# Optimization experiments

Hardware: AMD Instinct MI355X
Metric: run time of the kernel (lower is better)

The kernel has to match this reference:

```python
import jax, jax.numpy as jnp
from jax import lax
import numpy as np

D_MODEL = 1024
D_STATE = 16
D_CONV = 4
EXPAND = 2
D_INNER = EXPAND * D_MODEL          # 2048
DT_RANK = (D_MODEL + 15) // 16      # 64
B_SZ, SEQ = 2, 2048


def setup_inputs() -> dict:
    key = jax.random.key(0)
    ks = jax.random.split(key, 10)
    s = 0.02
    x = jax.random.normal(ks[0], (B_SZ, SEQ, D_MODEL), jnp.float32)
    ln_w = jnp.ones((D_MODEL,), jnp.float32)
    ln_b = jnp.zeros((D_MODEL,), jnp.float32)
    in_proj_w = jax.random.normal(ks[1], (2 * D_INNER, D_MODEL), jnp.float32) * s
    conv_w = jax.random.normal(ks[2], (D_INNER, 1, D_CONV), jnp.float32) * s
    conv_b = jnp.zeros((D_INNER,), jnp.float32)
    x_proj_w = jax.random.normal(ks[3], (DT_RANK + 2 * D_STATE, D_INNER), jnp.float32) * s
    dt_proj_w = jax.random.normal(ks[4], (D_INNER, DT_RANK), jnp.float32) * s
    dt_proj_b = jax.random.normal(ks[5], (D_INNER,), jnp.float32) * s
    # standard Mamba S4D-real init: A = -[1..d_state] per channel
    A_log = jnp.log(jnp.tile(jnp.arange(1, D_STATE + 1, dtype=jnp.float32), (D_INNER, 1)))
    D_param = jnp.ones((D_INNER,), jnp.float32)
    out_proj_w = jax.random.normal(ks[6], (D_MODEL, D_INNER), jnp.float32) * s
    return dict(x=x, ln_w=ln_w, ln_b=ln_b, in_proj_w=in_proj_w, conv_w=conv_w,
                conv_b=conv_b, x_proj_w=x_proj_w, dt_proj_w=dt_proj_w,
                dt_proj_b=dt_proj_b, A_log=A_log, D_param=D_param,
                out_proj_w=out_proj_w)


def _mamba_layer(x, ln_w, ln_b, in_proj_w, conv_w, conv_b, x_proj_w,
                 dt_proj_w, dt_proj_b, A_log, D_param, out_proj_w):
    # LayerNorm (eps=1e-5)
    mu = x.mean(-1, keepdims=True)
    var = ((x - mu) ** 2).mean(-1, keepdims=True)
    xn = (x - mu) * lax.rsqrt(var + 1e-5) * ln_w + ln_b

    # input projection -> gate + conv branch
    xz = jnp.einsum('bld,ed->ble', xn, in_proj_w)  # [B,L,2*D_INNER]
    x_in, z = jnp.split(xz, 2, axis=-1)

    # causal depthwise conv1d + SiLU
    xc = lax.conv_general_dilated(x_in.transpose(0, 2, 1), conv_w, (1,),
                                  [(D_CONV - 1, 0)],
                                  dimension_numbers=('NCH', 'OIH', 'NCH'),
                                  feature_group_count=D_INNER)
    xc = jax.nn.silu(xc + conv_b[None, :, None]).transpose(0, 2, 1)  # [B,L,D_INNER]

    # SSM parameters
    dbl = jnp.einsum('bld,ed->ble', xc, x_proj_w)  # [B,L,DT_RANK+2N]
    dt, Bm, Cm = jnp.split(dbl, [DT_RANK, DT_RANK + D_STATE], axis=-1)
    delta = jax.nn.softplus(jnp.einsum('blr,dr->bld', dt, dt_proj_w) + dt_proj_b)
    A = -jnp.exp(A_log)  # [D_INNER, D_STATE]

    # selective scan over time
    def step(h, inp):
        d_t, B_t, C_t, u_t = inp  # [B,D_INNER],[B,N],[B,N],[B,D_INNER]
        dA = jnp.exp(d_t[..., None] * A)                         # [B,D_INNER,N]
        h = dA * h + (d_t * u_t)[..., None] * B_t[:, None, :]    # [B,D_INNER,N]
        y = jnp.einsum('bdn,bn->bd', h, C_t)
        return h, y

    h0 = jnp.zeros((x.shape[0], D_INNER, D_STATE), x.dtype)
    _, ys = lax.scan(step, h0, (delta.transpose(1, 0, 2), Bm.transpose(1, 0, 2),
                                Cm.transpose(1, 0, 2), xc.transpose(1, 0, 2)))
    y = ys.transpose(1, 0, 2) + xc * D_param   # [B,L,D_INNER]

    y = y * jax.nn.silu(z)
    out = jnp.einsum('ble,de->bld', y, out_proj_w)
    # dropout p=0 (eval) -> identity; residual
    return x + out


def reference(x, ln_w, ln_b, in_proj_w, conv_w, conv_b, x_proj_w,
              dt_proj_w, dt_proj_b, A_log, D_param, out_proj_w):
    return _mamba_layer(x, ln_w, ln_b, in_proj_w, conv_w, conv_b, x_proj_w,
                        dt_proj_w, dt_proj_b, A_log, D_param, out_proj_w)
```

## Files before the change

### kernel.cpp

```cpp
#include <hip/hip_runtime.h>
#include <hip/hip_bf16.h>
#include <math.h>

#define D_MODEL 1024
#define D_INNER 2048
#define DT_RANK 64
#define D_STATE 16
#define BSZ 2
#define SEQ 2048
#define NROW (BSZ * SEQ)
#define NC 128
#define CL (SEQ / NC)
#define NCH (BSZ * D_INNER)
#define KSPLIT 16
#define KCH (D_INNER / KSPLIT)

typedef short bf16x8 __attribute__((ext_vector_type(8)));
typedef float f32x4 __attribute__((ext_vector_type(4)));

__device__ inline ushort f2bf(float f) {
    uint32_t u = __float_as_uint(f);
    return (ushort)((u + 0x7FFFu + ((u >> 16) & 1u)) >> 16);
}
__device__ inline float bf2f(ushort u) {
    return __uint_as_float(((uint32_t)u) << 16);
}

__device__ inline void gld_lds16(const void* g, void* l) {
    __builtin_amdgcn_global_load_lds(
        (__attribute__((address_space(1))) void*)g,
        (__attribute__((address_space(3))) void*)l, 16, 0, 0);
}

__global__ __launch_bounds__(256) void cvt_bf16(const float* __restrict__ in,
                                                ushort* __restrict__ out) {
    int i = blockIdx.x * 256 + threadIdx.x;
    float4 v = ((const float4*)in)[i];
    ushort4 o;
    o.x = f2bf(v.x); o.y = f2bf(v.y); o.z = f2bf(v.z); o.w = f2bf(v.w);
    ((ushort4*)out)[i] = o;
}

__global__ __launch_bounds__(256) void ln_kernel(const float* __restrict__ x,
                                                 const float* __restrict__ w,
                                                 const float* __restrict__ b,
                                                 ushort* __restrict__ xn) {
    int row = blockIdx.x;
    int tid = threadIdx.x;
    const float4* xr = (const float4*)(x + (size_t)row * D_MODEL);
    float4 v = xr[tid];
    float s  = v.x + v.y + v.z + v.w;
    float ss = v.x * v.x + v.y * v.y + v.z * v.z + v.w * v.w;
#pragma unroll
    for (int o = 32; o > 0; o >>= 1) {
        s  += __shfl_down(s, o);
        ss += __shfl_down(ss, o);
    }
    __shared__ float red[8];
    int wid = tid >> 6, lane = tid & 63;
    if (lane == 0) { red[wid] = s; red[4 + wid] = ss; }
    __syncthreads();
    s  = red[0] + red[1] + red[2] + red[3];
    ss = red[4] + red[5] + red[6] + red[7];
    float mu  = s * (1.0f / D_MODEL);
    float var = ss * (1.0f / D_MODEL) - mu * mu;
    float inv = rsqrtf(var + 1e-5f);
    float4 wv = ((const float4*)w)[tid];
    float4 bv = ((const float4*)b)[tid];
    ushort4 o4;
    o4.x = f2bf((v.x - mu) * inv * wv.x + bv.x);
    o4.y = f2bf((v.y - mu) * inv * wv.y + bv.y);
    o4.z = f2bf((v.z - mu) * inv * wv.z + bv.z);
    o4.w = f2bf((v.w - mu) * inv * wv.w + bv.w);
    ((ushort4*)(xn + (size_t)row * D_MODEL))[tid] = o4;
}

template <int MODE>
__global__ __launch_bounds__(256) void gemm_mfma(
    const ushort* __restrict__ A, int lda,
    const ushort* __restrict__ B, int ldb,
    float* __restrict__ C, ushort* __restrict__ Zb, int ldc, int splitN,
    const float* __restrict__ extra, int K) {
    __shared__ ushort lds[2][2][128 * 32];
    int tid = threadIdx.x;
    int w = tid >> 6, lane = tid & 63;
    int bm = blockIdx.y * 128, bn = blockIdx.x * 128;
    int wr = w >> 1, wc = w & 1;

    int srow = tid >> 2, sseg = (tid & 3) << 3;
    const ushort* Abase = A + (size_t)(bm + srow) * lda + sseg;
    const ushort* Bbase = B + (size_t)(bn + srow) * ldb + sseg;
    int l0 = w * 512;

    int frow = lane & 15, fk = (lane >> 4) << 3;
    f32x4 acc[4][4] = {};

#define STAGE(buf, k0)                                                        \
    do {                                                                      \
        gld_lds16(Abase + (k0),                     &lds[buf][0][l0]);        \
        gld_lds16(Abase + (size_t)64 * lda + (k0),  &lds[buf][0][2048 + l0]); \
        gld_lds16(Bbase + (k0),                     &lds[buf][1][l0]);        \
        gld_lds16(Bbase + (size_t)64 * ldb + (k0),  &lds[buf][1][2048 + l0]); \
    } while (0)

    int nk = K >> 5;
    int cur = 0;
    STAGE(0, 0);
    __syncthreads();
    for (int kt = 0; kt < nk; ++kt) {
        if (kt + 1 < nk) STAGE(cur ^ 1, (kt + 1) << 5);
        bf16x8 a[4], b[4];
#pragma unroll
        for (int m = 0; m < 4; ++m)
            a[m] = *(const bf16x8*)&lds[cur][0][(wr * 64 + m * 16 + frow) * 32 + fk];
#pragma unroll
        for (int n = 0; n < 4; ++n)
            b[n] = *(const bf16x8*)&lds[cur][1][(wc * 64 + n * 16 + frow) * 32 + fk];
#pragma unroll
        for (int m = 0; m < 4; ++m)
#pragma unroll
            for (int n = 0; n < 4; ++n)
                acc[m][n] = __builtin_amdgcn_mfma_f32_16x16x32_bf16(a[m], b[n], acc[m][n], 0, 0, 0);
        __syncthreads();
        cur ^= 1;
    }
#undef STAGE

    int rbase = bm + wr * 64 + ((lane >> 4) << 2);
    int cbase = bn + wc * 64 + (lane & 15);
#pragma unroll
    for (int m = 0; m < 4; ++m) {
#pragma unroll
        for (int n = 0; n < 4; ++n) {
            int gc = cbase + n * 16;
#pragma unroll
            for (int j = 0; j < 4; ++j) {
                int gr = rbase + m * 16 + j;
                float v = acc[m][n][j];
                if (MODE == 0) {
                    if (gc < splitN) C[(size_t)gr * ldc + gc] = v;
                    else             Zb[(size_t)gr * ldc + (gc - splitN)] = f2bf(v);
                } else {
                    C[(size_t)gr * ldc + gc] = v + extra[(size_t)gr * ldc + gc];
                }
            }
        }
    }
}

#define BM 64
#define BN 64
#define BK 16
template <int MODE>
__global__ __launch_bounds__(256) void gemm_tn(const float* __restrict__ A, int lda,
                                               const float* __restrict__ B, int ldb,
                                               float* __restrict__ C, int ldc,
                                               int M, int N, int K,
                                               const float* __restrict__ extra) {
    __shared__ float As[BK][BM];
    __shared__ float Bs[BK][BN];
    int bm = blockIdx.y * BM, bn = blockIdx.x * BN;
    int tid = threadIdx.x;
    int tx = tid & 15, ty = tid >> 4;
    int lrow = tid >> 2, lseg = (tid & 3) << 2;
    float acc[4][4] = {};

    for (int k0 = 0; k0 < K; k0 += BK) {
        float4 av = make_float4(0.f, 0.f, 0.f, 0.f);
        float4 bv = make_float4(0.f, 0.f, 0.f, 0.f);
        int agr = bm + lrow;
        if (agr < M) av = *(const float4*)(A + (size_t)agr * lda + k0 + lseg);
        int bgr = bn + lrow;
        if (bgr < N) bv = *(const float4*)(B + (size_t)bgr * ldb + k0 + lseg);
        __syncthreads();
        As[lseg + 0][lrow] = av.x; As[lseg + 1][lrow] = av.y;
        As[lseg + 2][lrow] = av.z; As[lseg + 3][lrow] = av.w;
        Bs[lseg + 0][lrow] = bv.x; Bs[lseg + 1][lrow] = bv.y;
        Bs[lseg + 2][lrow] = bv.z; Bs[lseg + 3][lrow] = bv.w;
        __syncthreads();
#pragma unroll
        for (int k = 0; k < BK; ++k) {
            float4 a4 = *(const float4*)&As[k][ty << 2];
            float4 b4 = *(const float4*)&Bs[k][tx << 2];
            float ar[4] = {a4.x, a4.y, a4.z, a4.w};
            float br[4] = {b4.x, b4.y, b4.z, b4.w};
#pragma unroll
            for (int i = 0; i < 4; ++i)
#pragma unroll
                for (int j = 0; j < 4; ++j) acc[i][j] += ar[i] * br[j];
        }
    }

#pragma unroll
    for (int i = 0; i < 4; ++i) {
        int gr = bm + (ty << 2) + i;
        if (gr >= M) continue;
#pragma unroll
        for (int j = 0; j < 4; ++j) {
            int gc = bn + (tx << 2) + j;
            if (gc >= N) continue;
            float v = acc[i][j];
            if (MODE == 1) {
                v += extra[gc];
                v = (v > 20.f) ? v : log1pf(expf(v));
                C[(size_t)gr * ldc + gc] = v;
            } else {
                C[(size_t)gr * ldc + gc] = v;
            }
        }
    }
}

__global__ __launch_bounds__(256) void gemm_b_split(const float* __restrict__ A,
                                                    const float* __restrict__ B,
                                                    float* __restrict__ part) {
    __shared__ float As[BK][BM];
    __shared__ float Bs[BK][BN];
    int bm = blockIdx.y * BM, bn = blockIdx.x * BN;
    int kc = blockIdx.z;
    int tid = threadIdx.x;
    int tx = tid & 15, ty = tid >> 4;
    int lrow = tid >> 2, lseg = (tid & 3) << 2;
    float acc[4][4] = {};

    int kbeg = kc * KCH;
    for (int k0 = kbeg; k0 < kbeg + KCH; k0 += BK) {
        float4 av = *(const float4*)(A + (size_t)(bm + lrow) * D_INNER + k0 + lseg);
        float4 bv = make_float4(0.f, 0.f, 0.f, 0.f);
        int bgr = bn + lrow;
        if (bgr < 96) bv = *(const float4*)(B + (size_t)bgr * D_INNER + k0 + lseg);
        __syncthreads();
        As[lseg + 0][lrow] = av.x; As[lseg + 1][lrow] = av.y;
        As[lseg + 2][lrow] = av.z; As[lseg + 3][lrow] = av.w;
        Bs[lseg + 0][lrow] = bv.x; Bs[lseg + 1][lrow] = bv.y;
        Bs[lseg + 2][lrow] = bv.z; Bs[lseg + 3][lrow] = bv.w;
        __syncthreads();
#pragma unroll
        for (int k = 0; k < BK; ++k) {
            float4 a4 = *(const float4*)&As[k][ty << 2];
            float4 b4 = *(const float4*)&Bs[k][tx << 2];
            float ar[4] = {a4.x, a4.y, a4.z, a4.w};
            float br[4] = {b4.x, b4.y, b4.z, b4.w};
#pragma unroll
            for (int i = 0; i < 4; ++i)
#pragma unroll
                for (int j = 0; j < 4; ++j) acc[i][j] += ar[i] * br[j];
        }
    }

    float* po = part + (size_t)kc * (NROW * 96);
#pragma unroll
    for (int i = 0; i < 4; ++i) {
        int gr = bm + (ty << 2) + i;
#pragma unroll
        for (int j = 0; j < 4; ++j) {
            int gc = bn + (tx << 2) + j;
            if (gc < 96) po[(size_t)gr * 96 + gc] = acc[i][j];
        }
    }
}

__global__ __launch_bounds__(256) void gemm_b_reduce(const float* __restrict__ part,
                                                     float* __restrict__ dbl) {
    int i = blockIdx.x * 256 + threadIdx.x;
    float s = 0.f;
#pragma unroll
    for (int kc = 0; kc < KSPLIT; ++kc)
        s += part[(size_t)kc * (NROW * 96) + i];
    dbl[i] = s;
}

__global__ __launch_bounds__(256) void conv_silu(const float* __restrict__ xin,
                                                 const float* __restrict__ w,
                                                 const float* __restrict__ cb,
                                                 float* __restrict__ xc) {
    int idx = blockIdx.x * 256 + threadIdx.x;
    int d4 = idx & 511;
    int m  = idx >> 9;
    int l  = m & (SEQ - 1);
    int d  = d4 << 2;
    float4 w0 = ((const float4*)w)[d + 0];
    float4 w1 = ((const float4*)w)[d + 1];
    float4 w2 = ((const float4*)w)[d + 2];
    float4 w3 = ((const float4*)w)[d + 3];
    float wr0[4] = {w0.x, w0.y, w0.z, w0.w};
    float wr1[4] = {w1.x, w1.y, w1.z, w1.w};
    float wr2[4] = {w2.x, w2.y, w2.z, w2.w};
    float wr3[4] = {w3.x, w3.y, w3.z, w3.w};
    float ax = cb[d], ay = cb[d + 1], az = cb[d + 2], aw = cb[d + 3];
#pragma unroll
    for (int j = 0; j < 4; ++j) {
        if (l - 3 + j >= 0) {
            float4 xv = *(const float4*)(xin + (size_t)(m - 3 + j) * D_INNER + d);
            ax += wr0[j] * xv.x;
            ay += wr1[j] * xv.y;
            az += wr2[j] * xv.z;
            aw += wr3[j] * xv.w;
        }
    }
    float4 o;
    o.x = ax / (1.f + __expf(-ax));
    o.y = ay / (1.f + __expf(-ay));
    o.z = az / (1.f + __expf(-az));
    o.w = aw / (1.f + __expf(-aw));
    *(float4*)(xc + (size_t)m * D_INNER + d) = o;
}

#define EXP4(e, cj) \
    e.x = __expf(dt * cj.x); e.y = __expf(dt * cj.y); \
    e.z = __expf(dt * cj.z); e.w = __expf(dt * cj.w);
#define HUPD(hj, cj, Bv) { float4 e; EXP4(e, cj) \
    hj.x = e.x * hj.x + du * Bv.x; hj.y = e.y * hj.y + du * Bv.y; \
    hj.z = e.z * hj.z + du * Bv.z; hj.w = e.w * hj.w + du * Bv.w; }

__global__ __launch_bounds__(256) void scan_phase1(const float* __restrict__ delta,
                                                   const float* __restrict__ xc,
                                                   const float* __restrict__ dbl,
                                                   const float* __restrict__ A_log,
                                                   float* __restrict__ S,
                                                   float* __restrict__ sumdt) {
    __shared__ float bs[CL][16];
    int tid = threadIdx.x;
    int g = blockIdx.x * 256 + tid;
    int c = g & (NCH - 1);
    int k = g >> 12;
    int d = c & (D_INNER - 1);
    int b = c >> 11;
    size_t r0 = (size_t)b * SEQ + (size_t)k * CL;

    if (tid < CL * 4) {
        int t = tid >> 2, j = (tid & 3) << 2;
        *(float4*)&bs[t][j] = *(const float4*)(dbl + (r0 + t) * 96 + DT_RANK + j);
    }

    const float4* al = (const float4*)(A_log + d * D_STATE);
    float4 c0 = al[0], c1 = al[1], c2 = al[2], c3 = al[3];
    c0.x = -__expf(c0.x); c0.y = -__expf(c0.y); c0.z = -__expf(c0.z); c0.w = -__expf(c0.w);
    c1.x = -__expf(c1.x); c1.y = -__expf(c1.y); c1.z = -__expf(c1.z); c1.w = -__expf(c1.w);
    c2.x = -__expf(c2.x); c2.y = -__expf(c2.y); c2.z = -__expf(c2.z); c2.w = -__expf(c2.w);
    c3.x = -__expf(c3.x); c3.y = -__expf(c3.y); c3.z = -__expf(c3.z); c3.w = -__expf(c3.w);
    __syncthreads();

    const float* pd = delta + r0 * D_INNER + d;
    const float* pu = xc    + r0 * D_INNER + d;
    float4 h0 = {}, h1 = {}, h2 = {}, h3 = {};
    float sdt = 0.f;
#pragma unroll 4
    for (int t = 0; t < CL; ++t) {
        float dt = *pd, u = *pu;
        float4 B0 = *(const float4*)&bs[t][0];
        float4 B1 = *(const float4*)&bs[t][4];
        float4 B2 = *(const float4*)&bs[t][8];
        float4 B3 = *(const float4*)&bs[t][12];
        float du = dt * u;
        sdt += dt;
        HUPD(h0, c0, B0) HUPD(h1, c1, B1) HUPD(h2, c2, B2) HUPD(h3, c3, B3)
        pd += D_INNER; pu += D_INNER;
    }
    float4* So = (float4*)(S + ((size_t)g << 4));
    So[0] = h0; So[1] = h1; So[2] = h2; So[3] = h3;
    sumdt[g] = sdt;
}

__global__ __launch_bounds__(256) void scan_phase2(float* __restrict__ S,
                                                   const float* __restrict__ sumdt,
                                                   const float* __restrict__ A_log) {
    int g = blockIdx.x * 256 + threadIdx.x;
    int n = g & 15;
    int c = g >> 4;
    int d = c & (D_INNER - 1);
    float cn = -__expf(A_log[d * D_STATE + n]);
    float h = 0.f;
#pragma unroll 8
    for (int k = 0; k < NC; ++k) {
        int kc = (k << 12) | c;
        float P = __expf(sumdt[kc] * cn);
        size_t o = ((size_t)kc << 4) + n;
        float s = S[o];
        S[o] = h;
        h = P * h + s;
    }
}

__global__ __launch_bounds__(256) void scan_phase3(const float* __restrict__ delta,
                                                   const float* __restrict__ xc,
                                                   const float* __restrict__ dbl,
                                                   const ushort* __restrict__ zb,
                                                   const float* __restrict__ A_log,
                                                   const float* __restrict__ Dp,
                                                   const float* __restrict__ hin,
                                                   ushort* __restrict__ y) {
    __shared__ float bcs[CL][32];
    int tid = threadIdx.x;
    int g = blockIdx.x * 256 + tid;
    int c = g & (NCH - 1);
    int k = g >> 12;
    int d = c & (D_INNER - 1);
    int b = c >> 11;
    size_t r0 = (size_t)b * SEQ + (size_t)k * CL;

    if (tid < CL * 8) {
        int t = tid >> 3, j = (tid & 7) << 2;
        *(float4*)&bcs[t][j] = *(const float4*)(dbl + (r0 + t) * 96 + DT_RANK + j);
    }

    const float4* al = (const float4*)(A_log + d * D_STATE);
    float4 c0 = al[0], c1 = al[1], c2 = al[2], c3 = al[3];
    c0.x = -__expf(c0.x); c0.y = -__expf(c0.y); c0.z = -__expf(c0.z); c0.w = -__expf(c0.w);
    c1.x = -__expf(c1.x); c1.y = -__expf(c1.y); c1.z = -__expf(c1.z); c1.w = -__expf(c1.w);
    c2.x = -__expf(c2.x); c2.y = -__expf(c2.y); c2.z = -__expf(c2.z); c2.w = -__expf(c2.w);
    c3.x = -__expf(c3.x); c3.y = -__expf(c3.y); c3.z = -__expf(c3.z); c3.w = -__expf(c3.w);
    float Dv = Dp[d];
    const float4* hi = (const float4*)(hin + ((size_t)g << 4));
    float4 h0 = hi[0], h1 = hi[1], h2 = hi[2], h3 = hi[3];
    __syncthreads();

    const float* pd = delta + r0 * D_INNER + d;
    const float* pu = xc    + r0 * D_INNER + d;
    const ushort* pz = zb   + r0 * D_INNER + d;
    ushort* py = y          + r0 * D_INNER + d;
#pragma unroll 4
    for (int t = 0; t < CL; ++t) {
        float dt = *pd, u = *pu;
        float4 B0 = *(const float4*)&bcs[t][0];
        float4 B1 = *(const float4*)&bcs[t][4];
        float4 B2 = *(const float4*)&bcs[t][8];
        float4 B3 = *(const float4*)&bcs[t][12];
        float4 C0 = *(const float4*)&bcs[t][16];
        float4 C1 = *(const float4*)&bcs[t][20];
        float4 C2 = *(const float4*)&bcs[t][24];
        float4 C3 = *(const float4*)&bcs[t][28];
        float du = dt * u;
        HUPD(h0, c0, B0) HUPD(h1, c1, B1) HUPD(h2, c2, B2) HUPD(h3, c3, B3)
        float acc = h0.x * C0.x + h0.y * C0.y + h0.z * C0.z + h0.w * C0.w
                  + h1.x * C1.x + h1.y * C1.y + h1.z * C1.z + h1.w * C1.w
                  + h2.x * C2.x + h2.y * C2.y + h2.z * C2.z + h2.w * C2.w
                  + h3.x * C3.x + h3.y * C3.y + h3.z * C3.z + h3.w * C3.w;
        float zv = bf2f(*pz);
        float sz = zv / (1.f + __expf(-zv));
        *py = f2bf((acc + u * Dv) * sz);
        pd += D_INNER; pu += D_INNER; pz += D_INNER; py += D_INNER;
    }
}

extern "C" void kernel_launch(void* const* d_in, const int* in_sizes, int n_in,
                              void* d_out, int out_size, void* d_ws, size_t ws_size,
                              hipStream_t stream) {
    const float* x       = (const float*)d_in[0];
    const float* ln_w    = (const float*)d_in[1];
    const float* ln_b    = (const float*)d_in[2];
    const float* in_proj = (const float*)d_in[3];
    const float* conv_w  = (const float*)d_in[4];
    const float* conv_b  = (const float*)d_in[5];
    const float* x_proj  = (const float*)d_in[6];
    const float* dt_w    = (const float*)d_in[7];
    const float* dt_b    = (const float*)d_in[8];
    const float* A_log   = (const float*)d_in[9];
    const float* Dp      = (const float*)d_in[10];
    const float* out_w   = (const float*)d_in[11];
    float* out = (float*)d_out;

    char* ws = (char*)d_ws;
    const size_t MB = 1024ull * 1024ull;
    ushort* xn_bf    = (ushort*)(ws);
    ushort* w_in_bf  = (ushort*)(ws + 8 * MB);
    float*  Shin     = (float*)(ws);
    float*  x_in     = (float*)(ws + 16 * MB);
    float*  part     = (float*)(ws + 16 * MB);
    ushort* w_out_bf = (ushort*)(ws + 41 * MB);
    float*  sumdt    = (float*)(ws + 45 * MB);
    ushort* zbuf_bf  = (ushort*)(ws + 48 * MB);
    float*  xc       = (float*)(ws + 64 * MB);
    float*  dbl      = (float*)(ws + 96 * MB);
    float*  delta    = (float*)(ws + 98 * MB);
    ushort* y_bf     = (ushort*)(ws + 130 * MB);

    cvt_bf16<<<(2 * D_INNER * D_MODEL / 4) / 256, 256, 0, stream>>>(in_proj, w_in_bf);

    ln_kernel<<<NROW, 256, 0, stream>>>(x, ln_w, ln_b, xn_bf);

    gemm_mfma<0><<<dim3(4096 / 128, NROW / 128), 256, 0, stream>>>(
        xn_bf, D_MODEL, w_in_bf, D_MODEL, x_in, zbuf_bf, D_INNER, D_INNER,
        nullptr, D_MODEL);

    conv_silu<<<(NROW * (D_INNER / 4)) / 256, 256, 0, stream>>>(x_in, conv_w, conv_b, xc);

    cvt_bf16<<<(D_MODEL * D_INNER / 4) / 256, 256, 0, stream>>>(out_w, w_out_bf);

    gemm_b_split<<<dim3(2, NROW / BM, KSPLIT), 256, 0, stream>>>(xc, x_proj, part);
    gemm_b_reduce<<<(NROW * 96) / 256, 256, 0, stream>>>(part, dbl);

    gemm_tn<1><<<dim3(D_INNER / BN, NROW / BM), 256, 0, stream>>>(
        dbl, 96, dt_w, DT_RANK, delta, D_INNER, NROW, D_INNER, DT_RANK, dt_b);

    scan_phase1<<<(NCH * NC) / 256, 256, 0, stream>>>(
        delta, xc, dbl, A_log, Shin, sumdt);
    scan_phase2<<<(NCH * D_STATE) / 256, 256, 0, stream>>>(Shin, sumdt, A_log);
    scan_phase3<<<(NCH * NC) / 256, 256, 0, stream>>>(
        delta, xc, dbl, zbuf_bf, A_log, Dp, Shin, y_bf);

    gemm_mfma<2><<<dim3(D_MODEL / 128, NROW / 128), 256, 0, stream>>>(
        y_bf, D_INNER, w_out_bf, D_INNER, out, nullptr, D_MODEL, 0,
        x, D_INNER);
}
```

Before: 408.6 us.

## Store intermediates in bf16 and move dt projection to MFMA GEMM

```diff
diff --git a/kernel.cpp b/kernel.cpp
--- a/kernel.cpp
+++ b/kernel.cpp
@@ -79,8 +79,8 @@
 __global__ __launch_bounds__(256) void gemm_mfma(
     const ushort* __restrict__ A, int lda,
     const ushort* __restrict__ B, int ldb,
-    float* __restrict__ C, ushort* __restrict__ Zb, int ldc, int splitN,
-    const float* __restrict__ extra, int K) {
+    float* __restrict__ C, ushort* __restrict__ Z0, ushort* __restrict__ Z1,
+    int ldc, int splitN, const float* __restrict__ extra, int K) {
     __shared__ ushort lds[2][2][128 * 32];
     int tid = threadIdx.x;
     int w = tid >> 6, lane = tid & 63;
@@ -138,8 +138,12 @@
                 int gr = rbase + m * 16 + j;
                 float v = acc[m][n][j];
                 if (MODE == 0) {
-                    if (gc < splitN) C[(size_t)gr * ldc + gc] = v;
-                    else             Zb[(size_t)gr * ldc + (gc - splitN)] = f2bf(v);
+                    if (gc < splitN) Z0[(size_t)gr * ldc + gc] = f2bf(v);
+                    else             Z1[(size_t)gr * ldc + (gc - splitN)] = f2bf(v);
+                } else if (MODE == 1) {
+                    v += extra[gc];
+                    v = (v > 20.f) ? v : log1pf(__expf(v));
+                    Z0[(size_t)gr * ldc + gc] = f2bf(v);
                 } else {
                     C[(size_t)gr * ldc + gc] = v + extra[(size_t)gr * ldc + gc];
                 }
@@ -151,67 +155,7 @@
 #define BM 64
 #define BN 64
 #define BK 16
-template <int MODE>
-__global__ __launch_bounds__(256) void gemm_tn(const float* __restrict__ A, int lda,
-                                               const float* __restrict__ B, int ldb,
-                                               float* __restrict__ C, int ldc,
-                                               int M, int N, int K,
-                                               const float* __restrict__ extra) {
-    __shared__ float As[BK][BM];
-    __shared__ float Bs[BK][BN];
-    int bm = blockIdx.y * BM, bn = blockIdx.x * BN;
-    int tid = threadIdx.x;
-    int tx = tid & 15, ty = tid >> 4;
-    int lrow = tid >> 2, lseg = (tid & 3) << 2;
-    float acc[4][4] = {};
-
-    for (int k0 = 0; k0 < K; k0 += BK) {
-        float4 av = make_float4(0.f, 0.f, 0.f, 0.f);
-        float4 bv = make_float4(0.f, 0.f, 0.f, 0.f);
-        int agr = bm + lrow;
-        if (agr < M) av = *(const float4*)(A + (size_t)agr * lda + k0 + lseg);
-        int bgr = bn + lrow;
-        if (bgr < N) bv = *(const float4*)(B + (size_t)bgr * ldb + k0 + lseg);
-        __syncthreads();
-        As[lseg + 0][lrow] = av.x; As[lseg + 1][lrow] = av.y;
-        As[lseg + 2][lrow] = av.z; As[lseg + 3][lrow] = av.w;
-        Bs[lseg + 0][lrow] = bv.x; Bs[lseg + 1][lrow] = bv.y;
-        Bs[lseg + 2][lrow] = bv.z; Bs[lseg + 3][lrow] = bv.w;
-        __syncthreads();
-#pragma unroll
-        for (int k = 0; k < BK; ++k) {
-            float4 a4 = *(const float4*)&As[k][ty << 2];
-            float4 b4 = *(const float4*)&Bs[k][tx << 2];
-            float ar[4] = {a4.x, a4.y, a4.z, a4.w};
-            float br[4] = {b4.x, b4.y, b4.z, b4.w};
-#pragma unroll
-            for (int i = 0; i < 4; ++i)
-#pragma unroll
-                for (int j = 0; j < 4; ++j) acc[i][j] += ar[i] * br[j];
-        }
-    }
-
-#pragma unroll
-    for (int i = 0; i < 4; ++i) {
-        int gr = bm + (ty << 2) + i;
-        if (gr >= M) continue;
-#pragma unroll
-        for (int j = 0; j < 4; ++j) {
-            int gc = bn + (tx << 2) + j;
-            if (gc >= N) continue;
-            float v = acc[i][j];
-            if (MODE == 1) {
-                v += extra[gc];
-                v = (v > 20.f) ? v : log1pf(expf(v));
-                C[(size_t)gr * ldc + gc] = v;
-            } else {
-                C[(size_t)gr * ldc + gc] = v;
-            }
-        }
-    }
-}
-
-__global__ __launch_bounds__(256) void gemm_b_split(const float* __restrict__ A,
+__global__ __launch_bounds__(256) void gemm_b_split(const ushort* __restrict__ A,
                                                     const float* __restrict__ B,
                                                     float* __restrict__ part) {
     __shared__ float As[BK][BM];
@@ -225,7 +169,8 @@
 
     int kbeg = kc * KCH;
     for (int k0 = kbeg; k0 < kbeg + KCH; k0 += BK) {
-        float4 av = *(const float4*)(A + (size_t)(bm + lrow) * D_INNER + k0 + lseg);
+        ushort4 au = *(const ushort4*)(A + (size_t)(bm + lrow) * D_INNER + k0 + lseg);
+        float4 av = make_float4(bf2f(au.x), bf2f(au.y), bf2f(au.z), bf2f(au.w));
         float4 bv = make_float4(0.f, 0.f, 0.f, 0.f);
         int bgr = bn + lrow;
         if (bgr < 96) bv = *(const float4*)(B + (size_t)bgr * D_INNER + k0 + lseg);
@@ -261,19 +206,19 @@
 }
 
 __global__ __launch_bounds__(256) void gemm_b_reduce(const float* __restrict__ part,
-                                                     float* __restrict__ dbl) {
+                                                     ushort* __restrict__ dbl) {
     int i = blockIdx.x * 256 + threadIdx.x;
     float s = 0.f;
 #pragma unroll
     for (int kc = 0; kc < KSPLIT; ++kc)
         s += part[(size_t)kc * (NROW * 96) + i];
-    dbl[i] = s;
-}
-
-__global__ __launch_bounds__(256) void conv_silu(const float* __restrict__ xin,
+    dbl[i] = f2bf(s);
+}
+
+__global__ __launch_bounds__(256) void conv_silu(const ushort* __restrict__ xin,
                                                  const float* __restrict__ w,
                                                  const float* __restrict__ cb,
-                                                 float* __restrict__ xc) {
+                                                 ushort* __restrict__ xc) {
     int idx = blockIdx.x * 256 + threadIdx.x;
     int d4 = idx & 511;
     int m  = idx >> 9;
@@ -291,19 +236,19 @@
 #pragma unroll
     for (int j = 0; j < 4; ++j) {
         if (l - 3 + j >= 0) {
-            float4 xv = *(const float4*)(xin + (size_t)(m - 3 + j) * D_INNER + d);
-            ax += wr0[j] * xv.x;
-            ay += wr1[j] * xv.y;
-            az += wr2[j] * xv.z;
-            aw += wr3[j] * xv.w;
+            ushort4 xu = *(const ushort4*)(xin + (size_t)(m - 3 + j) * D_INNER + d);
+            ax += wr0[j] * bf2f(xu.x);
+            ay += wr1[j] * bf2f(xu.y);
+            az += wr2[j] * bf2f(xu.z);
+            aw += wr3[j] * bf2f(xu.w);
         }
     }
-    float4 o;
-    o.x = ax / (1.f + __expf(-ax));
-    o.y = ay / (1.f + __expf(-ay));
-    o.z = az / (1.f + __expf(-az));
-    o.w = aw / (1.f + __expf(-aw));
-    *(float4*)(xc + (size_t)m * D_INNER + d) = o;
+    ushort4 o;
+    o.x = f2bf(ax / (1.f + __expf(-ax)));
+    o.y = f2bf(ay / (1.f + __expf(-ay)));
+    o.z = f2bf(az / (1.f + __expf(-az)));
+    o.w = f2bf(aw / (1.f + __expf(-aw)));
+    *(ushort4*)(xc + (size_t)m * D_INNER + d) = o;
 }
 
 #define EXP4(e, cj) \
@@ -313,9 +258,9 @@
     hj.x = e.x * hj.x + du * Bv.x; hj.y = e.y * hj.y + du * Bv.y; \
     hj.z = e.z * hj.z + du * Bv.z; hj.w = e.w * hj.w + du * Bv.w; }
 
-__global__ __launch_bounds__(256) void scan_phase1(const float* __restrict__ delta,
-                                                   const float* __restrict__ xc,
-                                                   const float* __restrict__ dbl,
+__global__ __launch_bounds__(256) void scan_phase1(const ushort* __restrict__ delta,
+                                                   const ushort* __restrict__ xc,
+                                                   const ushort* __restrict__ dbl,
                                                    const float* __restrict__ A_log,
                                                    float* __restrict__ S,
                                                    float* __restrict__ sumdt) {
@@ -330,7 +275,9 @@
 
     if (tid < CL * 4) {
         int t = tid >> 2, j = (tid & 3) << 2;
-        *(float4*)&bs[t][j] = *(const float4*)(dbl + (r0 + t) * 96 + DT_RANK + j);
+        ushort4 u4 = *(const ushort4*)(dbl + (r0 + t) * 96 + DT_RANK + j);
+        bs[t][j + 0] = bf2f(u4.x); bs[t][j + 1] = bf2f(u4.y);
+        bs[t][j + 2] = bf2f(u4.z); bs[t][j + 3] = bf2f(u4.w);
     }
 
     const float4* al = (const float4*)(A_log + d * D_STATE);
@@ -341,13 +288,13 @@
     c3.x = -__expf(c3.x); c3.y = -__expf(c3.y); c3.z = -__expf(c3.z); c3.w = -__expf(c3.w);
     __syncthreads();
 
-    const float* pd = delta + r0 * D_INNER + d;
-    const float* pu = xc    + r0 * D_INNER + d;
+    const ushort* pd = delta + r0 * D_INNER + d;
+    const ushort* pu = xc    + r0 * D_INNER + d;
     float4 h0 = {}, h1 = {}, h2 = {}, h3 = {};
     float sdt = 0.f;
 #pragma unroll 4
     for (int t = 0; t < CL; ++t) {
-        float dt = *pd, u = *pu;
+        float dt = bf2f(*pd), u = bf2f(*pu);
         float4 B0 = *(const float4*)&bs[t][0];
         float4 B1 = *(const float4*)&bs[t][4];
         float4 B2 = *(const float4*)&bs[t][8];
@@ -382,9 +329,9 @@
     }
 }
 
-__global__ __launch_bounds__(256) void scan_phase3(const float* __restrict__ delta,
-                                                   const float* __restrict__ xc,
-                                                   const float* __restrict__ dbl,
+__global__ __launch_bounds__(256) void scan_phase3(const ushort* __restrict__ delta,
+                                                   const ushort* __restrict__ xc,
+                                                   const ushort* __restrict__ dbl,
                                                    const ushort* __restrict__ zb,
                                                    const float* __restrict__ A_log,
                                                    const float* __restrict__ Dp,
@@ -401,7 +348,9 @@
 
     if (tid < CL * 8) {
         int t = tid >> 3, j = (tid & 7) << 2;
-        *(float4*)&bcs[t][j] = *(const float4*)(dbl + (r0 + t) * 96 + DT_RANK + j);
+        ushort4 u4 = *(const ushort4*)(dbl + (r0 + t) * 96 + DT_RANK + j);
+        bcs[t][j + 0] = bf2f(u4.x); bcs[t][j + 1] = bf2f(u4.y);
+        bcs[t][j + 2] = bf2f(u4.z); bcs[t][j + 3] = bf2f(u4.w);
     }
 
     const float4* al = (const float4*)(A_log + d * D_STATE);
@@ -415,13 +364,13 @@
     float4 h0 = hi[0], h1 = hi[1], h2 = hi[2], h3 = hi[3];
     __syncthreads();
 
-    const float* pd = delta + r0 * D_INNER + d;
-    const float* pu = xc    + r0 * D_INNER + d;
-    const ushort* pz = zb   + r0 * D_INNER + d;
-    ushort* py = y          + r0 * D_INNER + d;
+    const ushort* pd = delta + r0 * D_INNER + d;
+    const ushort* pu = xc    + r0 * D_INNER + d;
+    const ushort* pz = zb    + r0 * D_INNER + d;
+    ushort* py = y           + r0 * D_INNER + d;
 #pragma unroll 4
     for (int t = 0; t < CL; ++t) {
-        float dt = *pd, u = *pu;
+        float dt = bf2f(*pd), u = bf2f(*pu);
         float4 B0 = *(const float4*)&bcs[t][0];
         float4 B1 = *(const float4*)&bcs[t][4];
         float4 B2 = *(const float4*)&bcs[t][8];
@@ -465,41 +414,43 @@
     ushort* xn_bf    = (ushort*)(ws);
     ushort* w_in_bf  = (ushort*)(ws + 8 * MB);
     float*  Shin     = (float*)(ws);
-    float*  x_in     = (float*)(ws + 16 * MB);
-    float*  part     = (float*)(ws + 16 * MB);
-    ushort* w_out_bf = (ushort*)(ws + 41 * MB);
-    float*  sumdt    = (float*)(ws + 45 * MB);
-    ushort* zbuf_bf  = (ushort*)(ws + 48 * MB);
-    float*  xc       = (float*)(ws + 64 * MB);
-    float*  dbl      = (float*)(ws + 96 * MB);
-    float*  delta    = (float*)(ws + 98 * MB);
-    ushort* y_bf     = (ushort*)(ws + 130 * MB);
+    ushort* x_in_bf  = (ushort*)(ws + 16 * MB);
+    ushort* zbuf_bf  = (ushort*)(ws + 32 * MB);
+    ushort* xc_bf    = (ushort*)(ws + 48 * MB);
+    ushort* dbl_bf   = (ushort*)(ws + 64 * MB);
+    ushort* dt_w_bf  = (ushort*)(ws + 65 * MB);
+    ushort* delta_bf = (ushort*)(ws + 66 * MB);
+    ushort* y_bf     = (ushort*)(ws + 82 * MB);
+    float*  sumdt    = (float*)(ws + 98 * MB);
+    float*  part     = (float*)(ws + 100 * MB);
+    ushort* w_out_bf = (ushort*)(ws + 124 * MB);
 
     cvt_bf16<<<(2 * D_INNER * D_MODEL / 4) / 256, 256, 0, stream>>>(in_proj, w_in_bf);
+    cvt_bf16<<<(D_MODEL * D_INNER / 4) / 256, 256, 0, stream>>>(out_w, w_out_bf);
+    cvt_bf16<<<(D_INNER * DT_RANK / 4) / 256, 256, 0, stream>>>(dt_w, dt_w_bf);
 
     ln_kernel<<<NROW, 256, 0, stream>>>(x, ln_w, ln_b, xn_bf);
 
     gemm_mfma<0><<<dim3(4096 / 128, NROW / 128), 256, 0, stream>>>(
-        xn_bf, D_MODEL, w_in_bf, D_MODEL, x_in, zbuf_bf, D_INNER, D_INNER,
-        nullptr, D_MODEL);
-
-    conv_silu<<<(NROW * (D_INNER / 4)) / 256, 256, 0, stream>>>(x_in, conv_w, conv_b, xc);
-
-    cvt_bf16<<<(D_MODEL * D_INNER / 4) / 256, 256, 0, stream>>>(out_w, w_out_bf);
-
-    gemm_b_split<<<dim3(2, NROW / BM, KSPLIT), 256, 0, stream>>>(xc, x_proj, part);
-    gemm_b_reduce<<<(NROW * 96) / 256, 256, 0, stream>>>(part, dbl);
-
-    gemm_tn<1><<<dim3(D_INNER / BN, NROW / BM), 256, 0, stream>>>(
-        dbl, 96, dt_w, DT_RANK, delta, D_INNER, NROW, D_INNER, DT_RANK, dt_b);
+        xn_bf, D_MODEL, w_in_bf, D_MODEL, nullptr, x_in_bf, zbuf_bf,
+        D_INNER, D_INNER, nullptr, D_MODEL);
+
+    conv_silu<<<(NROW * (D_INNER / 4)) / 256, 256, 0, stream>>>(x_in_bf, conv_w, conv_b, xc_bf);
+
+    gemm_b_split<<<dim3(2, NROW / BM, KSPLIT), 256, 0, stream>>>(xc_bf, x_proj, part);
+    gemm_b_reduce<<<(NROW * 96) / 256, 256, 0, stream>>>(part, dbl_bf);
+
+    gemm_mfma<1><<<dim3(D_INNER / 128, NROW / 128), 256, 0, stream>>>(
+        dbl_bf, 96, dt_w_bf, DT_RANK, nullptr, delta_bf, nullptr,
+        D_INNER, 0, dt_b, DT_RANK);
 
     scan_phase1<<<(NCH * NC) / 256, 256, 0, stream>>>(
-        delta, xc, dbl, A_log, Shin, sumdt);
+        delta_bf, xc_bf, dbl_bf, A_log, Shin, sumdt);
     scan_phase2<<<(NCH * D_STATE) / 256, 256, 0, stream>>>(Shin, sumdt, A_log);
     scan_phase3<<<(NCH * NC) / 256, 256, 0, stream>>>(
-        delta, xc, dbl, zbuf_bf, A_log, Dp, Shin, y_bf);
+        delta_bf, xc_bf, dbl_bf, zbuf_bf, A_log, Dp, Shin, y_bf);
 
     gemm_mfma<2><<<dim3(D_MODEL / 128, NROW / 128), 256, 0, stream>>>(
-        y_bf, D_INNER, w_out_bf, D_INNER, out, nullptr, D_MODEL, 0,
-        x, D_INNER);
-}
+        y_bf, D_INNER, w_out_bf, D_INNER, out, nullptr, nullptr,
+        D_MODEL, 0, x, D_INNER);
+}
```

Result: faster. 396.2 us (-3.0%).
